# Performance work log

Hardware: AMD Instinct MI355X
Metric: run time of the kernel (lower is better)

Reference implementation:

```python
import jax, jax.numpy as jnp
import numpy as np

GRID_SIZE = 16
SPLINE_ORDER = 4
GRID_LO, GRID_HI = -1.0, 1.0
NUM_GRID = 2 * SPLINE_ORDER + GRID_SIZE + 1  # 25 knots
NUM_COEFFS = GRID_SIZE + SPLINE_ORDER        # 20 basis functions
B, IN_F, OUT_F = 2048, 512, 512


def _make_grid():
    h = (GRID_HI - GRID_LO) / GRID_SIZE
    t1 = -SPLINE_ORDER * h + GRID_LO
    t2 = (GRID_SIZE + SPLINE_ORDER + 1) * h + GRID_LO
    return jnp.linspace(t1, t2, NUM_GRID)


def _bspline_basis(x, grid):
    # x: [..., in]; returns [..., in, NUM_COEFFS] via De Boor recursion
    xe = x[..., None]
    bases = ((xe >= grid[:-1]) & (xe < grid[1:])).astype(x.dtype)
    for k in range(1, SPLINE_ORDER + 1):
        left = (xe - grid[:-k - 1]) / (grid[k:-1] - grid[:-k - 1]) * bases[..., :-1]
        right = (grid[k + 1:] - xe) / (grid[k + 1:] - grid[1:-k]) * bases[..., 1:]
        bases = left + right
    return bases


def setup_inputs() -> dict:
    key = jax.random.key(0)
    ks = jax.random.split(key, 5)
    fan = np.sqrt(1.0 / IN_F)
    return {
        "x": jax.random.normal(ks[0], (B, IN_F), jnp.float32),
        "prelu_weight": jax.random.normal(ks[1], (OUT_F, IN_F), jnp.float32) * 0.25,
        "base_weight": jax.random.uniform(ks[2], (OUT_F, IN_F), jnp.float32, -fan, fan),
        "spline_weight": jax.random.uniform(ks[3], (OUT_F, IN_F), jnp.float32, -fan, fan),
        "spline_coeffs": jax.random.normal(ks[4], (OUT_F, IN_F, NUM_COEFFS), jnp.float32) * 0.1,
    }


def reference(x, prelu_weight, base_weight, spline_weight, spline_coeffs):
    grid = _make_grid()
    xc = jnp.clip(x, GRID_LO, GRID_HI)
    pos = jax.nn.relu(xc)
    neg = xc - pos
    # base path: sum_j base_w[i,j]*(prelu_w[i,j]*neg[b,j] + pos[b,j])
    # fused: never materialize the [out, B, in] prelu output
    base = neg @ (base_weight * prelu_weight).T + pos @ base_weight.T  # [B, out]
    basis = _bspline_basis(xc, grid)  # [B, in, K]
    # spline path: fold spline_weight into coeffs, single contraction over (j,k)
    eff_coeffs = spline_weight[:, :, None] * spline_coeffs  # [out, in, K]
    spline = jnp.einsum('bjk,ijk->bi', basis, eff_coeffs)   # [B, out]
    return base + spline
```

## Files before the change

kernel.cpp:

```cpp
#include <hip/hip_runtime.h>


typedef _Float16 half_t;
typedef __attribute__((ext_vector_type(8))) _Float16 half8;
typedef __attribute__((ext_vector_type(4))) float floatx4;

#define B_DIM   2048
#define J_DIM   512
#define O_DIM   512
#define SLOTS   22
#define K_TOT   (J_DIM * SLOTS)
#define MTILE   128
#define NTILE   64
#define BK      32
#define KSPLIT  11
#define KS_LEN  (K_TOT / KSPLIT)
#define KCH     (KS_LEN / BK)
#define ZERO_BLKS 64

__device__ __forceinline__ void bspline5(float xc, int& k0, float Nv[5]) {
    const float invS = 7.68f;
    float u = (xc + 1.5f) * invS;
    int m = (int)u;
    m = min(max(m, 3), 19);
    k0 = m - 4;
    Nv[0] = 1.f; Nv[1] = 0.f; Nv[2] = 0.f; Nv[3] = 0.f; Nv[4] = 0.f;
#pragma unroll
    for (int d = 1; d <= 4; ++d) {
        float nw[5];
        float inv_d = 1.0f / (float)d;
#pragma unroll
        for (int r = 0; r < 5; ++r) {
            if (r > d) { nw[r] = 0.f; continue; }
            float kk = (float)(m - d + r);
            float acc = 0.f;
            if (r >= 1) acc += (u - kk) * Nv[r - 1];
            if (r < d)  acc += (kk + (float)(d + 1) - u) * Nv[r];
            nw[r] = acc * inv_d;
        }
#pragma unroll
        for (int r = 0; r < 5; ++r) Nv[r] = nw[r];
    }
}

__global__ __launch_bounds__(256) void prep_all(const float* __restrict__ x,
                                                const float* __restrict__ pw,
                                                const float* __restrict__ bw,
                                                const float* __restrict__ sw,
                                                const float* __restrict__ sc,
                                                half_t* __restrict__ A,
                                                half_t* __restrict__ Ct,
                                                float* __restrict__ out) {
    __shared__ half_t rec[J_DIM * SLOTS];
    int bid = blockIdx.x;
    int t = threadIdx.x;

    if (bid < ZERO_BLKS) {
        float4* o = (float4*)out;
        int base = bid * 4096;
#pragma unroll
        for (int i = 0; i < 16; ++i)
            o[base + i * 256 + t] = make_float4(0.f, 0.f, 0.f, 0.f);
        return;
    }

    if (bid < ZERO_BLKS + O_DIM) {
        int i = bid - ZERO_BLKS;
#pragma unroll
        for (int jj = 0; jj < 2; ++jj) {
            int j = t + jj * 256;
            size_t ij = (size_t)i * J_DIM + j;
            float s = sw[ij], b = bw[ij], p = pw[ij];
            const float4* scp4 = (const float4*)(sc + ij * 20);
            half_t* r = rec + j * SLOTS;
#pragma unroll
            for (int v = 0; v < 5; ++v) {
                float4 c4 = scp4[v];
                r[v * 4 + 0] = (half_t)(s * c4.x);
                r[v * 4 + 1] = (half_t)(s * c4.y);
                r[v * 4 + 2] = (half_t)(s * c4.z);
                r[v * 4 + 3] = (half_t)(s * c4.w);
            }
            r[20] = (half_t)(b * p);
            r[21] = (half_t)b;
        }
        __syncthreads();
        const uint4* src = (const uint4*)rec;
        uint4* dst = (uint4*)(Ct + (size_t)i * K_TOT);
        for (int idx = t; idx < (J_DIM * SLOTS * 2) / 16; idx += 256) dst[idx] = src[idx];
        return;
    }

    int b = bid - ZERO_BLKS - O_DIM;
#pragma unroll
    for (int jj = 0; jj < 2; ++jj) {
        int j = t + jj * 256;
        float xv = x[(size_t)b * J_DIM + j];
        float xc = fminf(fmaxf(xv, -1.f), 1.f);
        float pos = fmaxf(xc, 0.f);
        float neg = xc - pos;
        int k0; float Nv[5];
        bspline5(xc, k0, Nv);
        half_t* r = rec + j * SLOTS;
#pragma unroll
        for (int k = 0; k < 20; ++k) r[k] = (half_t)0.f;
#pragma unroll
        for (int rr = 0; rr < 5; ++rr) {
            int k = k0 + rr;
            if (k >= 0) r[k] = (half_t)Nv[rr];
        }
        r[20] = (half_t)neg;
        r[21] = (half_t)pos;
    }
    __syncthreads();
    const uint4* src = (const uint4*)rec;
    uint4* dst = (uint4*)(A + (size_t)b * K_TOT);
    for (int i = t; i < (J_DIM * SLOTS * 2) / 16; i += 256) dst[i] = src[i];
}

__global__ __launch_bounds__(256, 6) void gemm_f16(const half_t* __restrict__ A,
                                                   const half_t* __restrict__ Bt,
                                                   float* __restrict__ out) {
    __shared__ half_t As[2][MTILE * BK];
    __shared__ half_t Bs[2][NTILE * BK];

    int m0 = blockIdx.x * MTILE;
    int n0 = blockIdx.y * NTILE;
    int ks = blockIdx.z * KS_LEN;

    int t = threadIdx.x;
    int w = t >> 6;
    int l = t & 63;

    floatx4 acc[2][4] = {};

    int lrow = l >> 2;
    int lkof = (((l & 3) ^ ((l >> 3) & 3)) * 8);

    const half_t* gA = A + (size_t)m0 * K_TOT + ks;
    const half_t* gB = Bt + (size_t)n0 * K_TOT + ks;

    int q = l >> 4;
    int fr = l & 15;
    int qs = (q ^ ((fr >> 1) & 3)) * 8;

#define ISSUE_LOADS(c, p)                                                     \
    {                                                                         \
        int kb = (c) * BK;                                                    \
        _Pragma("unroll")                                                     \
        for (int n = 0; n < 2; ++n) {                                         \
            int r = w * 32 + n * 16 + lrow;                                   \
            __builtin_amdgcn_global_load_lds(                                 \
                (const __attribute__((address_space(1))) unsigned int*)       \
                    (gA + (size_t)r * K_TOT + kb + lkof),                     \
                (__attribute__((address_space(3))) unsigned int*)             \
                    (&As[p][0] + w * 1024 + n * 512),                         \
                16, 0, 0);                                                    \
        }                                                                     \
        {                                                                     \
            int r = w * 16 + lrow;                                            \
            __builtin_amdgcn_global_load_lds(                                 \
                (const __attribute__((address_space(1))) unsigned int*)       \
                    (gB + (size_t)r * K_TOT + kb + lkof),                     \
                (__attribute__((address_space(3))) unsigned int*)             \
                    (&Bs[p][0] + w * 512),                                    \
                16, 0, 0);                                                    \
        }                                                                     \
    }

    ISSUE_LOADS(0, 0)
    int p = 0;
    for (int c = 0; c < KCH; ++c) {
        __syncthreads();
        if (c + 1 < KCH) ISSUE_LOADS(c + 1, p ^ 1)

        half8 af[2], bf[4];
#pragma unroll
        for (int mt = 0; mt < 2; ++mt)
            af[mt] = *(const half8*)(&As[p][0] + (w * 32 + mt * 16 + fr) * BK + qs);
#pragma unroll
        for (int nt = 0; nt < 4; ++nt)
            bf[nt] = *(const half8*)(&Bs[p][0] + (nt * 16 + fr) * BK + qs);
#pragma unroll
        for (int mt = 0; mt < 2; ++mt)
#pragma unroll
            for (int nt = 0; nt < 4; ++nt)
                acc[mt][nt] = __builtin_amdgcn_mfma_f32_16x16x32_f16(
                    af[mt], bf[nt], acc[mt][nt], 0, 0, 0);
        p ^= 1;
    }
#undef ISSUE_LOADS

#pragma unroll
    for (int mt = 0; mt < 2; ++mt)
#pragma unroll
        for (int nt = 0; nt < 4; ++nt) {
            int rr = m0 + w * 32 + mt * 16 + q * 4;
            int cc = n0 + nt * 16 + fr;
#pragma unroll
            for (int r = 0; r < 4; ++r)
                atomicAdd(out + (size_t)(rr + r) * O_DIM + cc, acc[mt][nt][r]);
        }
}

__global__ __launch_bounds__(256) void kan_fallback(const float* __restrict__ x,
                                                    const float* __restrict__ pw,
                                                    const float* __restrict__ bw,
                                                    const float* __restrict__ sw,
                                                    const float* __restrict__ sc,
                                                    float* __restrict__ out) {
    __shared__ float s_neg[J_DIM], s_pos[J_DIM], s_bas[J_DIM][5];
    __shared__ int s_k0[J_DIM];
    int b = blockIdx.x;
    int t = threadIdx.x;
#pragma unroll
    for (int jj = 0; jj < 2; ++jj) {
        int j = t + jj * 256;
        float xv = x[(size_t)b * J_DIM + j];
        float xc = fminf(fmaxf(xv, -1.f), 1.f);
        float pos = fmaxf(xc, 0.f);
        s_pos[j] = pos;
        s_neg[j] = xc - pos;
        int k0; float Nv[5];
        bspline5(xc, k0, Nv);
        s_k0[j] = k0;
#pragma unroll
        for (int r = 0; r < 5; ++r) s_bas[j][r] = Nv[r];
    }
    __syncthreads();
    for (int i = t; i < O_DIM; i += 256) {
        float acc = 0.f;
        for (int j = 0; j < J_DIM; ++j) {
            size_t ij = (size_t)i * J_DIM + j;
            float bwv = bw[ij];
            acc += bwv * (pw[ij] * s_neg[j] + s_pos[j]);
            int k0 = s_k0[j];
            const float* cp = sc + ij * 20;
            float sp = 0.f;
#pragma unroll
            for (int r = 0; r < 5; ++r) {
                int k = k0 + r;
                if (k >= 0) sp += s_bas[j][r] * cp[k];
            }
            acc += sw[ij] * sp;
        }
        out[(size_t)b * O_DIM + i] = acc;
    }
}

extern "C" void kernel_launch(void* const* d_in, const int* in_sizes, int n_in,
                              void* d_out, int out_size, void* d_ws, size_t ws_size,
                              hipStream_t stream) {
    const float* x  = (const float*)d_in[0];
    const float* pw = (const float*)d_in[1];
    const float* bw = (const float*)d_in[2];
    const float* sw = (const float*)d_in[3];
    const float* sc = (const float*)d_in[4];
    float* out = (float*)d_out;

    const size_t ws_needed = (size_t)(B_DIM + O_DIM) * K_TOT * sizeof(half_t);
    if (ws_size < ws_needed) {
        kan_fallback<<<B_DIM, 256, 0, stream>>>(x, pw, bw, sw, sc, out);
        return;
    }

    half_t* A  = (half_t*)d_ws;
    half_t* Ct = A + (size_t)B_DIM * K_TOT;

    prep_all<<<ZERO_BLKS + O_DIM + B_DIM, 256, 0, stream>>>(x, pw, bw, sw, sc, A, Ct, out);
    dim3 g(B_DIM / MTILE, O_DIM / NTILE, KSPLIT);
    gemm_f16<<<g, 256, 0, stream>>>(A, Ct, out);
}
```

Before: 147.6 us.

## Load MFMA fragments directly from global into registers, bypassing LDS

The shared-memory double buffer fed by global_load_lds is replaced with direct per-lane half8 loads from global memory into MFMA operand registers. Two chunks are prefetched ahead in a register pipeline, and the __syncthreads barriers are gone. The occupancy hint in launch_bounds drops from 6 to 3 to make room for the extra live registers. In exchange, the four waves no longer share B tiles through LDS, so each wave fetches the same B fragments redundantly. The global accesses also become narrower 64-byte row segments.

```diff
diff --git a/kernel.cpp b/kernel.cpp
--- a/kernel.cpp
+++ b/kernel.cpp
@@ -118,12 +118,9 @@
     for (int i = t; i < (J_DIM * SLOTS * 2) / 16; i += 256) dst[i] = src[i];
 }
 
-__global__ __launch_bounds__(256, 6) void gemm_f16(const half_t* __restrict__ A,
+__global__ __launch_bounds__(256, 3) void gemm_f16(const half_t* __restrict__ A,
                                                    const half_t* __restrict__ Bt,
                                                    float* __restrict__ out) {
-    __shared__ half_t As[2][MTILE * BK];
-    __shared__ half_t Bs[2][NTILE * BK];
-
     int m0 = blockIdx.x * MTILE;
     int n0 = blockIdx.y * NTILE;
     int ks = blockIdx.z * KS_LEN;
@@ -131,65 +128,53 @@
     int t = threadIdx.x;
     int w = t >> 6;
     int l = t & 63;
+    int fr = l & 15;
+    int q  = l >> 4;
+
+    const size_t rs16 = (size_t)16 * K_TOT;
+    const half_t* pa = A  + (size_t)(m0 + w * 32 + fr) * K_TOT + ks + q * 8;
+    const half_t* pb = Bt + (size_t)(n0 + fr)          * K_TOT + ks + q * 8;
 
     floatx4 acc[2][4] = {};
 
-    int lrow = l >> 2;
-    int lkof = (((l & 3) ^ ((l >> 3) & 3)) * 8);
-
-    const half_t* gA = A + (size_t)m0 * K_TOT + ks;
-    const half_t* gB = Bt + (size_t)n0 * K_TOT + ks;
-
-    int q = l >> 4;
-    int fr = l & 15;
-    int qs = (q ^ ((fr >> 1) & 3)) * 8;
-
-#define ISSUE_LOADS(c, p)                                                     \
+#define LOADSET(da, db, kb)                                                   \
     {                                                                         \
-        int kb = (c) * BK;                                                    \
         _Pragma("unroll")                                                     \
-        for (int n = 0; n < 2; ++n) {                                         \
-            int r = w * 32 + n * 16 + lrow;                                   \
-            __builtin_amdgcn_global_load_lds(                                 \
-                (const __attribute__((address_space(1))) unsigned int*)       \
-                    (gA + (size_t)r * K_TOT + kb + lkof),                     \
-                (__attribute__((address_space(3))) unsigned int*)             \
-                    (&As[p][0] + w * 1024 + n * 512),                         \
-                16, 0, 0);                                                    \
-        }                                                                     \
-        {                                                                     \
-            int r = w * 16 + lrow;                                            \
-            __builtin_amdgcn_global_load_lds(                                 \
-                (const __attribute__((address_space(1))) unsigned int*)       \
-                    (gB + (size_t)r * K_TOT + kb + lkof),                     \
-                (__attribute__((address_space(3))) unsigned int*)             \
-                    (&Bs[p][0] + w * 512),                                    \
-                16, 0, 0);                                                    \
-        }                                                                     \
-    }
-
-    ISSUE_LOADS(0, 0)
-    int p = 0;
-    for (int c = 0; c < KCH; ++c) {
-        __syncthreads();
-        if (c + 1 < KCH) ISSUE_LOADS(c + 1, p ^ 1)
-
-        half8 af[2], bf[4];
-#pragma unroll
-        for (int mt = 0; mt < 2; ++mt)
-            af[mt] = *(const half8*)(&As[p][0] + (w * 32 + mt * 16 + fr) * BK + qs);
-#pragma unroll
-        for (int nt = 0; nt < 4; ++nt)
-            bf[nt] = *(const half8*)(&Bs[p][0] + (nt * 16 + fr) * BK + qs);
-#pragma unroll
-        for (int mt = 0; mt < 2; ++mt)
-#pragma unroll
-            for (int nt = 0; nt < 4; ++nt)
-                acc[mt][nt] = __builtin_amdgcn_mfma_f32_16x16x32_f16(
-                    af[mt], bf[nt], acc[mt][nt], 0, 0, 0);
-        p ^= 1;
-    }
-#undef ISSUE_LOADS
+        for (int mt = 0; mt < 2; ++mt)                                        \
+            da[mt] = *(const half8*)(pa + mt * rs16 + (kb));                  \
+        _Pragma("unroll")                                                     \
+        for (int nt = 0; nt < 4; ++nt)                                        \
+            db[nt] = *(const half8*)(pb + nt * rs16 + (kb));                  \
+    }
+
+#define MFMA8(sa, sb)                                                         \
+    {                                                                         \
+        _Pragma("unroll")                                                     \
+        for (int mt = 0; mt < 2; ++mt)                                        \
+            _Pragma("unroll")                                                 \
+            for (int nt = 0; nt < 4; ++nt)                                    \
+                acc[mt][nt] = __builtin_amdgcn_mfma_f32_16x16x32_f16(         \
+                    sa[mt], sb[nt], acc[mt][nt], 0, 0, 0);                    \
+    }
+
+    half8 a0[2], b0[4], a1[2], b1[4];
+    LOADSET(a0, b0, 0)
+    LOADSET(a1, b1, BK)
+
+#pragma unroll 1
+    for (int c = 0; c < KCH; c += 2) {
+        half8 a2[2], b2[4], a3[2], b3[4];
+        if (c + 2 < KCH) LOADSET(a2, b2, (c + 2) * BK)
+        MFMA8(a0, b0)
+        if (c + 3 < KCH) LOADSET(a3, b3, (c + 3) * BK)
+        MFMA8(a1, b1)
+#pragma unroll
+        for (int mt = 0; mt < 2; ++mt) { a0[mt] = a2[mt]; a1[mt] = a3[mt]; }
+#pragma unroll
+        for (int nt = 0; nt < 4; ++nt) { b0[nt] = b2[nt]; b1[nt] = b3[nt]; }
+    }
+#undef LOADSET
+#undef MFMA8
 
 #pragma unroll
     for (int mt = 0; mt < 2; ++mt)
```

Result: slower. 222.6 us (+50.8%).
